# Kernel optimization log

Measured on AMD Instinct MI355X. Metric: run time of the kernel, lower is better.

## Reference

```python
import jax, jax.numpy as jnp
import numpy as np

P = 16; H_IMG = 384; W_IMG = 384; D = 1024
N_LAYERS = 24; DI = 2048; DS = 16; DTR = 64; DC = 4; EPS = 1e-5


def setup_inputs() -> dict:
    key = jax.random.key(0)
    ks = jax.random.split(key, 12)
    B = 2
    inp = {}
    inp["x"] = jax.random.normal(ks[0], (B, 3, H_IMG, W_IMG), jnp.float32)
    inp["patch_w"] = jax.random.normal(ks[1], (D, 3, P, P), jnp.float32) * 0.02
    inp["patch_b"] = jnp.zeros((D,), jnp.float32)
    inp["pos_embed"] = jax.random.normal(ks[2], (1, (H_IMG // P) * (W_IMG // P), D), jnp.float32) * 0.02
    inp["ln_g"] = jnp.ones((N_LAYERS, D), jnp.float32)
    inp["ln_b"] = jnp.zeros((N_LAYERS, D), jnp.float32)
    inp["in_w"] = jax.random.normal(ks[3], (N_LAYERS, 2 * DI, D), jnp.float32) * 0.02
    inp["conv_w"] = jax.random.normal(ks[4], (N_LAYERS, DI, DC), jnp.float32) * 0.1
    inp["conv_b"] = jnp.zeros((N_LAYERS, DI), jnp.float32)
    inp["xproj_w"] = jax.random.normal(ks[5], (N_LAYERS, DTR + 2 * DS, DI), jnp.float32) * 0.02
    inp["dt_w"] = jax.random.normal(ks[6], (N_LAYERS, DI, DTR), jnp.float32) * 0.02
    inp["dt_b"] = jnp.full((N_LAYERS, DI), -4.0, jnp.float32)  # softplus(-4) ~ 0.018
    inp["A_log"] = jnp.broadcast_to(jnp.log(jnp.arange(1, DS + 1, dtype=jnp.float32)), (N_LAYERS, DI, DS)).copy()
    inp["D_param"] = jnp.ones((N_LAYERS, DI), jnp.float32)
    inp["out_w"] = jax.random.normal(ks[7], (N_LAYERS, D, DI), jnp.float32) * 0.02
    return inp


def _layer_norm(x, g, b):
    mu = jnp.mean(x, axis=-1, keepdims=True)
    var = jnp.var(x, axis=-1, keepdims=True)
    return (x - mu) * jax.lax.rsqrt(var + EPS) * g + b


def _mamba_block(x, p):
    g, bn, Win, Wc, bc, Wxp, Wdt, bdt, Alog, Dd, Wout = p
    u = _layer_norm(x, g, bn)                          # [B,L,D]
    xz = jnp.einsum('bld,ed->ble', u, Win)             # [B,L,2*DI]
    xi, z = jnp.split(xz, 2, axis=-1)
    # causal depthwise conv1d along L (kernel DC=4)
    xt = jnp.moveaxis(xi, 1, 2)                        # [B,DI,L]
    L = xt.shape[-1]
    xpad = jnp.pad(xt, ((0, 0), (0, 0), (DC - 1, 0)))
    xc = sum(Wc[:, k][None, :, None] * xpad[:, :, k:k + L] for k in range(DC)) + bc[None, :, None]
    xc = jax.nn.silu(jnp.moveaxis(xc, 1, 2))           # [B,L,DI]
    dbc = jnp.einsum('bld,ed->ble', xc, Wxp)           # [B,L,DTR+2*DS]
    dt, Bm, Cm = jnp.split(dbc, [DTR, DTR + DS], axis=-1)
    dt = jax.nn.softplus(jnp.einsum('blr,dr->bld', dt, Wdt) + bdt)  # [B,L,DI]
    A = -jnp.exp(Alog)                                 # [DI,DS]
    dA = jnp.exp(dt[..., None] * A)                    # [B,L,DI,DS]
    dBx = (dt * xc)[..., None] * Bm[:, :, None, :]     # [B,L,DI,DS]

    def step(h, inp):
        dA_t, dBx_t, C_t = inp
        h = dA_t * h + dBx_t                           # [B,DI,DS]
        y = jnp.einsum('bds,bs->bd', h, C_t)
        return h, y

    h0 = jnp.zeros((x.shape[0], DI, DS), x.dtype)
    xs = (jnp.moveaxis(dA, 1, 0), jnp.moveaxis(dBx, 1, 0), jnp.moveaxis(Cm, 1, 0))
    _, ys = jax.lax.scan(step, h0, xs)                 # ys: [L,B,DI]
    y = jnp.moveaxis(ys, 0, 1) + Dd * xc
    y = y * jax.nn.silu(z)
    return x + jnp.einsum('ble,de->bld', y, Wout)


def _forward(x, patch_w, patch_b, pos_embed, ln_g, ln_b, in_w, conv_w, conv_b,
             xproj_w, dt_w, dt_b, A_log, D_param, out_w):
    feat = jax.lax.conv_general_dilated(
        x, patch_w, (P, P), 'VALID',
        dimension_numbers=('NCHW', 'OIHW', 'NCHW')) + patch_b[None, :, None, None]
    Bn, Dd, Hh, Ww = feat.shape
    tok = feat.reshape(Bn, Dd, Hh * Ww).transpose(0, 2, 1)  # [B,L,D]
    h0, w0 = H_IMG // P, W_IMG // P
    pe = pos_embed.reshape(1, h0, w0, Dd)
    pe = jax.image.resize(pe, (1, Hh, Ww, Dd), 'bilinear')  # align_corners=False
    tok = tok + pe.reshape(1, Hh * Ww, Dd)
    params = (ln_g, ln_b, in_w, conv_w, conv_b, xproj_w, dt_w, dt_b, A_log, D_param, out_w)

    def layer(carry, p):
        return jax.checkpoint(_mamba_block)(carry, p), None

    tok, _ = jax.lax.scan(layer, tok, params)
    return tok


def reference(x, patch_w, patch_b, pos_embed, ln_g, ln_b, in_w, conv_w, conv_b,
              xproj_w, dt_w, dt_b, A_log, D_param, out_w):
    return _forward(x, patch_w, patch_b, pos_embed, ln_g, ln_b, in_w, conv_w, conv_b,
                    xproj_w, dt_w, dt_b, A_log, D_param, out_w)
```

## Files before the change

kernel.cpp:

```cpp
#include <hip/hip_runtime.h>
#include <hip/hip_bf16.h>
#include <math.h>

#define PATCH   16
#define HIMG    384
#define WIMG    384
#define DMODEL  1024
#define NLAYERS 24
#define DI      2048
#define DSTATE  16
#define DTR     64
#define DC      4
#define LN_EPS  1e-5f
#define BATCH   2
#define GRIDTOK 24
#define LTOK    (GRIDTOK*GRIDTOK)
#define NTOK    (BATCH*LTOK)
#define KPATCH  (3*PATCH*PATCH)
#define NCH     16
#define LC      (LTOK/NCH)
#define PSTRIDE ((size_t)NTOK * 2 * DI)
#define XP_SK   16

typedef __attribute__((ext_vector_type(8))) short short8;
typedef __attribute__((ext_vector_type(4))) float f32x4;

__device__ __forceinline__ float sigmoidf_(float v) { return 1.f / (1.f + __expf(-v)); }
__device__ __forceinline__ unsigned short f2bf(float f) {
    __hip_bfloat16 h = __float2bfloat16(f);
    return *(unsigned short*)&h;
}

__device__ __forceinline__ int xcd_swizzle(int orig, int nwg) {
    const int q = nwg >> 3, r = nwg & 7;
    const int xcd = orig & 7, idx = orig >> 3;
    return (xcd < r ? xcd * (q + 1) : r * (q + 1) + (xcd - r) * q) + idx;
}
__device__ __forceinline__ void swz_xyz(int& bx, int& by, int& bz) {
    const int gx = gridDim.x, gy = gridDim.y;
    const int nwg = gx * gy * gridDim.z;
    const int orig = blockIdx.x + gx * (blockIdx.y + gy * blockIdx.z);
    const int id = xcd_swizzle(orig, nwg);
    bx = id % gx;
    const int rest = id / gx;
    by = rest % gy;
    bz = rest / gy;
}

__global__ void f2bf_kernel(const float* __restrict__ in, unsigned short* __restrict__ out, int n4) {
    for (int i = blockIdx.x * blockDim.x + threadIdx.x; i < n4; i += gridDim.x * blockDim.x) {
        const float4 v = ((const float4*)in)[i];
        ushort4 o;
        o.x = f2bf(v.x); o.y = f2bf(v.y); o.z = f2bf(v.z); o.w = f2bf(v.w);
        ((ushort4*)out)[i] = o;
    }
}

__global__ void im2col_kernel(const float* __restrict__ x, unsigned short* __restrict__ xcol) {
    int idx = blockIdx.x * blockDim.x + threadIdx.x;
    if (idx >= NTOK * KPATCH) return;
    int t = idx / KPATCH, k = idx % KPATCH;
    int b = t / LTOK, hw = t % LTOK;
    int h = hw / GRIDTOK, w = hw % GRIDTOK;
    int c = k / (PATCH*PATCH), r = k % (PATCH*PATCH);
    int i = r / PATCH, j = r % PATCH;
    xcol[idx] = f2bf(x[(((size_t)(b*3 + c)*HIMG) + h*PATCH + i)*WIMG + w*PATCH + j]);
}

__global__ __launch_bounds__(256) void layernorm_kernel(
        const float* __restrict__ x, const float* __restrict__ g,
        const float* __restrict__ b, unsigned short* __restrict__ u) {
    const int t = blockIdx.x;
    const int tid = threadIdx.x;
    const float4 xv = ((const float4*)(x + (size_t)t * DMODEL))[tid];
    float s = xv.x + xv.y + xv.z + xv.w;
    float q = xv.x*xv.x + xv.y*xv.y + xv.z*xv.z + xv.w*xv.w;
    #pragma unroll
    for (int off = 32; off >= 1; off >>= 1) {
        s += __shfl_xor(s, off);
        q += __shfl_xor(q, off);
    }
    __shared__ float red[8];
    if ((tid & 63) == 0) { red[tid >> 6] = s; red[4 + (tid >> 6)] = q; }
    __syncthreads();
    s = red[0] + red[1] + red[2] + red[3];
    q = red[4] + red[5] + red[6] + red[7];
    const float mu   = s * (1.f / DMODEL);
    const float var  = q * (1.f / DMODEL) - mu * mu;
    const float rstd = rsqrtf(var + LN_EPS);
    const float4 gv = ((const float4*)g)[tid];
    const float4 bv = ((const float4*)b)[tid];
    ushort4 o;
    o.x = f2bf((xv.x - mu) * rstd * gv.x + bv.x);
    o.y = f2bf((xv.y - mu) * rstd * gv.y + bv.y);
    o.z = f2bf((xv.z - mu) * rstd * gv.z + bv.z);
    o.w = f2bf((xv.w - mu) * rstd * gv.w + bv.w);
    ((ushort4*)(u + (size_t)t * DMODEL))[tid] = o;
}

__global__ __launch_bounds__(256) void gemm_mfma_bt(
        const unsigned short* __restrict__ A, int lda,
        const float* __restrict__ B, int ldb,
        float* __restrict__ C, int M, int N, int Ksub) {
    __shared__ unsigned short As[128 * 64];
    __shared__ unsigned short Bs[128 * 64];
    int bx, by, bz;
    swz_xyz(bx, by, bz);
    const int tid = threadIdx.x;
    const int m0 = bx * 128;
    const int n0 = by * 128;
    const int koff = bz * Ksub;
    C += (size_t)bz * M * N;

    const int lane = tid & 63;
    const int wid  = tid >> 6;
    const int wm = (wid >> 1) * 64;
    const int wn = (wid & 1) * 64;
    const int fr = lane & 15;
    const int cb = lane >> 4;

    const int srow = tid >> 3;
    const int skc  = tid & 7;

    f32x4 acc[4][4];
    #pragma unroll
    for (int i = 0; i < 4; ++i)
        #pragma unroll
        for (int j = 0; j < 4; ++j) acc[i][j] = (f32x4){0.f, 0.f, 0.f, 0.f};

    uint4  areg[4];
    float4 breg[4][2];

    const int nk = Ksub / 64;
    #pragma unroll
    for (int i = 0; i < 4; ++i) {
        const int r = srow + 32 * i;
        areg[i] = *(const uint4*)(A + (size_t)(m0 + r) * lda + koff + skc * 8);
        const float* bp = B + (size_t)(n0 + r) * ldb + koff + skc * 8;
        breg[i][0] = *(const float4*)bp;
        breg[i][1] = *(const float4*)(bp + 4);
    }

    for (int ks = 0; ks < nk; ++ks) {
        __syncthreads();
        #pragma unroll
        for (int i = 0; i < 4; ++i) {
            const int r = srow + 32 * i;
            const int idx = r * 64 + ((skc ^ (r & 7)) << 3);
            *(uint4*)&As[idx] = areg[i];
            const float* bf = (const float*)&breg[i][0];
            short8 hv;
            #pragma unroll
            for (int j = 0; j < 8; ++j) hv[j] = (short)f2bf(bf[j]);
            *(short8*)&Bs[idx] = hv;
        }
        __syncthreads();
        if (ks + 1 < nk) {
            const int k1 = koff + (ks + 1) * 64;
            #pragma unroll
            for (int i = 0; i < 4; ++i) {
                const int r = srow + 32 * i;
                areg[i] = *(const uint4*)(A + (size_t)(m0 + r) * lda + k1 + skc * 8);
                const float* bp = B + (size_t)(n0 + r) * ldb + k1 + skc * 8;
                breg[i][0] = *(const float4*)bp;
                breg[i][1] = *(const float4*)(bp + 4);
            }
        }
        #pragma unroll
        for (int kk = 0; kk < 2; ++kk) {
            short8 af[4], bfr[4];
            #pragma unroll
            for (int mi = 0; mi < 4; ++mi) {
                const int row = wm + mi * 16 + fr;
                af[mi] = *(const short8*)&As[row * 64 + (((kk * 4 + cb) ^ (row & 7)) << 3)];
            }
            #pragma unroll
            for (int ni = 0; ni < 4; ++ni) {
                const int row = wn + ni * 16 + fr;
                bfr[ni] = *(const short8*)&Bs[row * 64 + (((kk * 4 + cb) ^ (row & 7)) << 3)];
            }
            #pragma unroll
            for (int mi = 0; mi < 4; ++mi)
                #pragma unroll
                for (int ni = 0; ni < 4; ++ni)
                    acc[mi][ni] = __builtin_amdgcn_mfma_f32_16x16x32_bf16(
                        af[mi], bfr[ni], acc[mi][ni], 0, 0, 0);
        }
    }

    #pragma unroll
    for (int mi = 0; mi < 4; ++mi) {
        const int rbase = m0 + wm + mi * 16 + cb * 4;
        #pragma unroll
        for (int ni = 0; ni < 4; ++ni) {
            const int col = n0 + wn + ni * 16 + fr;
            #pragma unroll
            for (int j = 0; j < 4; ++j)
                C[(size_t)(rbase + j) * N + col] = acc[mi][ni][j];
        }
    }
}

template<int EPI>
__global__ __launch_bounds__(256) void gemm_bb(
        const unsigned short* __restrict__ A, int lda,
        const unsigned short* __restrict__ B, int ldb,
        float* __restrict__ C, int M, int N, int Ksub,
        const float* __restrict__ bias, const float* __restrict__ aux) {
    __shared__ unsigned short As[128 * 64];
    __shared__ unsigned short Bs[128 * 64];
    int bx, by, bz;
    swz_xyz(bx, by, bz);
    const int tid = threadIdx.x;
    const int m0 = bx * 128;
    const int n0 = by * 128;

    const int lane = tid & 63;
    const int wid  = tid >> 6;
    const int wm = (wid >> 1) * 64;
    const int wn = (wid & 1) * 64;
    const int fr = lane & 15;
    const int cb = lane >> 4;
    const int srow = tid >> 3;
    const int skc  = tid & 7;

    f32x4 acc[4][4];
    #pragma unroll
    for (int i = 0; i < 4; ++i)
        #pragma unroll
        for (int j = 0; j < 4; ++j) acc[i][j] = (f32x4){0.f, 0.f, 0.f, 0.f};

    uint4 areg[4], breg[4];
    const int nk = Ksub / 64;
    #pragma unroll
    for (int i = 0; i < 4; ++i) {
        const int r = srow + 32 * i;
        areg[i] = *(const uint4*)(A + (size_t)(m0 + r) * lda + skc * 8);
        breg[i] = *(const uint4*)(B + (size_t)(n0 + r) * ldb + skc * 8);
    }

    for (int ks = 0; ks < nk; ++ks) {
        __syncthreads();
        #pragma unroll
        for (int i = 0; i < 4; ++i) {
            const int r = srow + 32 * i;
            const int idx = r * 64 + ((skc ^ (r & 7)) << 3);
            *(uint4*)&As[idx] = areg[i];
            *(uint4*)&Bs[idx] = breg[i];
        }
        __syncthreads();
        if (ks + 1 < nk) {
            const int k1 = (ks + 1) * 64;
            #pragma unroll
            for (int i = 0; i < 4; ++i) {
                const int r = srow + 32 * i;
                areg[i] = *(const uint4*)(A + (size_t)(m0 + r) * lda + k1 + skc * 8);
                breg[i] = *(const uint4*)(B + (size_t)(n0 + r) * ldb + k1 + skc * 8);
            }
        }
        #pragma unroll
        for (int kk = 0; kk < 2; ++kk) {
            short8 af[4], bfr[4];
            #pragma unroll
            for (int mi = 0; mi < 4; ++mi) {
                const int row = wm + mi * 16 + fr;
                af[mi] = *(const short8*)&As[row * 64 + (((kk * 4 + cb) ^ (row & 7)) << 3)];
            }
            #pragma unroll
            for (int ni = 0; ni < 4; ++ni) {
                const int row = wn + ni * 16 + fr;
                bfr[ni] = *(const short8*)&Bs[row * 64 + (((kk * 4 + cb) ^ (row & 7)) << 3)];
            }
            #pragma unroll
            for (int mi = 0; mi < 4; ++mi)
                #pragma unroll
                for (int ni = 0; ni < 4; ++ni)
                    acc[mi][ni] = __builtin_amdgcn_mfma_f32_16x16x32_bf16(
                        af[mi], bfr[ni], acc[mi][ni], 0, 0, 0);
        }
    }

    #pragma unroll
    for (int mi = 0; mi < 4; ++mi) {
        const int rbase = m0 + wm + mi * 16 + cb * 4;
        #pragma unroll
        for (int ni = 0; ni < 4; ++ni) {
            const int col = n0 + wn + ni * 16 + fr;
            #pragma unroll
            for (int j = 0; j < 4; ++j) {
                float v = acc[mi][ni][j];
                if (EPI == 2)
                    v += bias[col] + aux[(size_t)((rbase + j) % LTOK) * DMODEL + col];
                C[(size_t)(rbase + j) * N + col] = v;
            }
        }
    }
}

__global__ __launch_bounds__(256) void gemm_xproj64(
        const unsigned short* __restrict__ A,
        const unsigned short* __restrict__ B,
        float* __restrict__ C) {
    __shared__ unsigned short As[64 * 64];
    __shared__ unsigned short Bs[96 * 64];
    int bx, by, bz;
    swz_xyz(bx, by, bz);
    const int tid = threadIdx.x;
    const int m0 = bx * 64;
    const int koff = by * (DI / XP_SK);
    C += (size_t)by * NTOK * 96;

    const int lane = tid & 63;
    const int wid  = tid >> 6;
    const int wm = wid * 16;
    const int fr = lane & 15;
    const int cb = lane >> 4;
    const int srow = tid >> 3;
    const int skc  = tid & 7;

    f32x4 acc[6];
    #pragma unroll
    for (int j = 0; j < 6; ++j) acc[j] = (f32x4){0.f, 0.f, 0.f, 0.f};

    uint4 areg[2], breg[3];
    areg[0] = *(const uint4*)(A + (size_t)(m0 + srow) * DI + koff + skc * 8);
    areg[1] = *(const uint4*)(A + (size_t)(m0 + srow + 32) * DI + koff + skc * 8);
    #pragma unroll
    for (int i = 0; i < 3; ++i) {
        const int idx = tid + 256 * i;
        breg[i] = *(const uint4*)(B + (size_t)(idx >> 3) * DI + koff + (idx & 7) * 8);
    }

    const int nk = (DI / XP_SK) / 64;
    for (int ks = 0; ks < nk; ++ks) {
        __syncthreads();
        {
            const int r0 = srow, r1 = srow + 32;
            *(uint4*)&As[r0 * 64 + ((skc ^ (r0 & 7)) << 3)] = areg[0];
            *(uint4*)&As[r1 * 64 + ((skc ^ (r1 & 7)) << 3)] = areg[1];
        }
        #pragma unroll
        for (int i = 0; i < 3; ++i) {
            const int idx = tid + 256 * i;
            const int r = idx >> 3, kc = idx & 7;
            *(uint4*)&Bs[r * 64 + ((kc ^ (r & 7)) << 3)] = breg[i];
        }
        __syncthreads();
        if (ks + 1 < nk) {
            const int k1 = koff + (ks + 1) * 64;
            areg[0] = *(const uint4*)(A + (size_t)(m0 + srow) * DI + k1 + skc * 8);
            areg[1] = *(const uint4*)(A + (size_t)(m0 + srow + 32) * DI + k1 + skc * 8);
            #pragma unroll
            for (int i = 0; i < 3; ++i) {
                const int idx = tid + 256 * i;
                breg[i] = *(const uint4*)(B + (size_t)(idx >> 3) * DI + k1 + (idx & 7) * 8);
            }
        }
        #pragma unroll
        for (int kk = 0; kk < 2; ++kk) {
            const int arow = wm + fr;
            const short8 af = *(const short8*)&As[arow * 64 + (((kk * 4 + cb) ^ (arow & 7)) << 3)];
            short8 bfr[6];
            #pragma unroll
            for (int ni = 0; ni < 6; ++ni) {
                const int row = ni * 16 + fr;
                bfr[ni] = *(const short8*)&Bs[row * 64 + (((kk * 4 + cb) ^ (row & 7)) << 3)];
            }
            #pragma unroll
            for (int ni = 0; ni < 6; ++ni)
                acc[ni] = __builtin_amdgcn_mfma_f32_16x16x32_bf16(af, bfr[ni], acc[ni], 0, 0, 0);
        }
    }

    const int rbase = m0 + wm + cb * 4;
    #pragma unroll
    for (int ni = 0; ni < 6; ++ni) {
        const int col = ni * 16 + fr;
        #pragma unroll
        for (int j = 0; j < 4; ++j)
            C[(size_t)(rbase + j) * 96 + col] = acc[ni][j];
    }
}

__global__ __launch_bounds__(256) void gemm_dt(
        const unsigned short* __restrict__ A,
        const unsigned short* __restrict__ B,
        float* __restrict__ C, const float* __restrict__ bias) {
    __shared__ unsigned short As[128 * 64];
    __shared__ unsigned short Bs[64 * 64];
    int bx, by, bz;
    swz_xyz(bx, by, bz);
    const int tid = threadIdx.x;
    const int m0 = bx * 128;
    const int n0 = by * 64;

    const int lane = tid & 63;
    const int wid  = tid >> 6;
    const int wm = (wid >> 1) * 64;
    const int wn = (wid & 1) * 32;
    const int fr = lane & 15;
    const int cb = lane >> 4;
    const int srow = tid >> 3;
    const int skc  = tid & 7;

    #pragma unroll
    for (int i = 0; i < 4; ++i) {
        const int r = srow + 32 * i;
        const uint4 v = *(const uint4*)(A + (size_t)(m0 + r) * 64 + skc * 8);
        *(uint4*)&As[r * 64 + ((skc ^ (r & 7)) << 3)] = v;
    }
    #pragma unroll
    for (int i = 0; i < 2; ++i) {
        const int r = srow + 32 * i;
        const uint4 v = *(const uint4*)(B + (size_t)(n0 + r) * 64 + skc * 8);
        *(uint4*)&Bs[r * 64 + ((skc ^ (r & 7)) << 3)] = v;
    }
    __syncthreads();

    f32x4 acc[4][2];
    #pragma unroll
    for (int i = 0; i < 4; ++i)
        #pragma unroll
        for (int j = 0; j < 2; ++j) acc[i][j] = (f32x4){0.f, 0.f, 0.f, 0.f};

    #pragma unroll
    for (int kk = 0; kk < 2; ++kk) {
        short8 af[4], bfr[2];
        #pragma unroll
        for (int mi = 0; mi < 4; ++mi) {
            const int row = wm + mi * 16 + fr;
            af[mi] = *(const short8*)&As[row * 64 + (((kk * 4 + cb) ^ (row & 7)) << 3)];
        }
        #pragma unroll
        for (int ni = 0; ni < 2; ++ni) {
            const int row = wn + ni * 16 + fr;
            bfr[ni] = *(const short8*)&Bs[row * 64 + (((kk * 4 + cb) ^ (row & 7)) << 3)];
        }
        #pragma unroll
        for (int mi = 0; mi < 4; ++mi)
            #pragma unroll
            for (int ni = 0; ni < 2; ++ni)
                acc[mi][ni] = __builtin_amdgcn_mfma_f32_16x16x32_bf16(
                    af[mi], bfr[ni], acc[mi][ni], 0, 0, 0);
    }

    #pragma unroll
    for (int mi = 0; mi < 4; ++mi) {
        const int rbase = m0 + wm + mi * 16 + cb * 4;
        #pragma unroll
        for (int ni = 0; ni < 2; ++ni) {
            const int col = n0 + wn + ni * 16 + fr;
            #pragma unroll
            for (int j = 0; j < 4; ++j) {
                float v = acc[mi][ni][j] + bias[col];
                v = (v > 20.f) ? v : log1pf(__expf(v));
                C[(size_t)(rbase + j) * DI + col] = v;
            }
        }
    }
}

__global__ void reduce16_kernel(const float* __restrict__ part, float* __restrict__ out,
                                unsigned short* __restrict__ out64, int n) {
    int i = blockIdx.x * blockDim.x + threadIdx.x;
    if (i >= n) return;
    float s = 0.f;
    #pragma unroll
    for (int z = 0; z < XP_SK; ++z) s += part[(size_t)z * n + i];
    out[i] = s;
    const int col = i % 96;
    if (col < 64) out64[(i / 96) * 64 + col] = f2bf(s);
}

__global__ void conv1d_silu_kernel(const float* __restrict__ xzP,
                                   const float* __restrict__ wc,
                                   const float* __restrict__ bc,
                                   float* __restrict__ xc,
                                   unsigned short* __restrict__ xc_bf) {
    int idx = blockIdx.x * blockDim.x + threadIdx.x;
    if (idx >= NTOK * DI) return;
    const int t = idx >> 11;
    const int e = idx & (DI - 1);
    const int l = t % LTOK;
    const float4 w = *(const float4*)(wc + e * DC);
    const float* xp0 = xzP + (size_t)t * (2*DI) + e;
    const float* xp1 = xp0 + PSTRIDE;
    float acc = bc[e] + w.w * (xp0[0] + xp1[0]);
    if (l >= 1) acc += w.z * (xp0[-(2*DI)]   + xp1[-(2*DI)]);
    if (l >= 2) acc += w.y * (xp0[-2*(2*DI)] + xp1[-2*(2*DI)]);
    if (l >= 3) acc += w.x * (xp0[-3*(2*DI)] + xp1[-3*(2*DI)]);
    const float r = acc * sigmoidf_(acc);
    xc[idx] = r;
    xc_bf[idx] = f2bf(r);
}

__global__ __launch_bounds__(256) void scan_pass1(
        const float* __restrict__ dt, const float* __restrict__ xc,
        const float* __restrict__ dbc, const float* __restrict__ Alog,
        float* __restrict__ Fst, float* __restrict__ sdt) {
    const int tid = threadIdx.x;
    const int e  = blockIdx.x * 256 + tid;
    const int c  = blockIdx.y;
    const int b  = blockIdx.z;
    const int l0 = c * LC;
    const size_t tb = (size_t)b * LTOK + l0;

    __shared__ float Bs[LC][16];
    for (int idx = tid; idx < LC * 16; idx += 256) {
        const int row = idx >> 4, s = idx & 15;
        Bs[row][s] = dbc[(tb + row) * 96 + 64 + s];
    }

    float Aval[DSTATE];
    {
        const float* ap = Alog + (size_t)e * DSTATE;
        #pragma unroll
        for (int s = 0; s < DSTATE; ++s) Aval[s] = -__expf(ap[s]);
    }
    __syncthreads();

    const float* dtp = dt + tb * DI + e;
    const float* xcp = xc + tb * DI + e;
    float h[DSTATE];
    #pragma unroll
    for (int s = 0; s < DSTATE; ++s) h[s] = 0.f;
    float sum_dt = 0.f;

    float dtv = dtp[0], xcv = xcp[0];
    for (int l = 0; l < LC; ++l) {
        float dtn = 0.f, xcn = 0.f;
        if (l + 1 < LC) { dtn = dtp[(size_t)(l+1) * DI]; xcn = xcp[(size_t)(l+1) * DI]; }
        sum_dt += dtv;
        const float dx = dtv * xcv;
        const float4* brow = (const float4*)&Bs[l][0];
        const float4 b0 = brow[0], b1 = brow[1], b2 = brow[2], b3 = brow[3];
        const float bb[16] = {b0.x,b0.y,b0.z,b0.w, b1.x,b1.y,b1.z,b1.w,
                              b2.x,b2.y,b2.z,b2.w, b3.x,b3.y,b3.z,b3.w};
        #pragma unroll
        for (int s = 0; s < DSTATE; ++s)
            h[s] = fmaf(__expf(dtv * Aval[s]), h[s], dx * bb[s]);
        dtv = dtn; xcv = xcn;
    }

    float4* Fp = (float4*)(Fst + ((((size_t)b * NCH + c) * DI) + e) * DSTATE);
    #pragma unroll
    for (int q = 0; q < 4; ++q)
        Fp[q] = make_float4(h[q*4+0], h[q*4+1], h[q*4+2], h[q*4+3]);
    sdt[((size_t)b * NCH + c) * DI + e] = sum_dt;
}

__global__ __launch_bounds__(256) void scan_pass3(
        const float* __restrict__ dt, const float* __restrict__ xc,
        const float* __restrict__ dbc, const float* __restrict__ xzP,
        const float* __restrict__ Alog, const float* __restrict__ Dp,
        const float* __restrict__ Fst, const float* __restrict__ sdt,
        unsigned short* __restrict__ y) {
    const int tid = threadIdx.x;
    const int e  = blockIdx.x * 256 + tid;
    const int c  = blockIdx.y;
    const int b  = blockIdx.z;
    const int l0 = c * LC;
    const size_t tb = (size_t)b * LTOK + l0;

    __shared__ float BCs[LC][32];
    for (int idx = tid; idx < LC * 32; idx += 256) {
        const int row = idx >> 5, col = idx & 31;
        BCs[row][col] = dbc[(tb + row) * 96 + 64 + col];
    }

    float Aval[DSTATE];
    {
        const float* ap = Alog + (size_t)e * DSTATE;
        #pragma unroll
        for (int s = 0; s < DSTATE; ++s) Aval[s] = -__expf(ap[s]);
    }
    const float Dv = Dp[e];

    float h[DSTATE];
    #pragma unroll
    for (int s = 0; s < DSTATE; ++s) h[s] = 0.f;
    for (int c2 = 0; c2 < c; ++c2) {
        const size_t base = ((size_t)b * NCH + c2) * DI + e;
        const float sd = sdt[base];
        const float4* Fp = (const float4*)(Fst + base * DSTATE);
        const float4 f0 = Fp[0], f1 = Fp[1], f2 = Fp[2], f3 = Fp[3];
        const float ff[16] = {f0.x,f0.y,f0.z,f0.w, f1.x,f1.y,f1.z,f1.w,
                              f2.x,f2.y,f2.z,f2.w, f3.x,f3.y,f3.z,f3.w};
        #pragma unroll
        for (int s = 0; s < DSTATE; ++s)
            h[s] = fmaf(__expf(Aval[s] * sd), h[s], ff[s]);
    }
    __syncthreads();

    const float* dtp = dt + tb * DI + e;
    const float* xcp = xc + tb * DI + e;
    const float* zp0 = xzP + tb * (2*DI) + DI + e;
    const float* zp1 = zp0 + PSTRIDE;
    unsigned short* yp = y + tb * DI + e;

    float dtv = dtp[0], xcv = xcp[0], zv = zp0[0] + zp1[0];
    for (int l = 0; l < LC; ++l) {
        float dtn = 0.f, xcn = 0.f, zn = 0.f;
        if (l + 1 < LC) {
            dtn = dtp[(size_t)(l+1) * DI];
            xcn = xcp[(size_t)(l+1) * DI];
            zn  = zp0[(size_t)(l+1) * (2*DI)] + zp1[(size_t)(l+1) * (2*DI)];
        }
        const float dx = dtv * xcv;
        const float4* brow = (const float4*)&BCs[l][0];
        const float4 b0 = brow[0], b1 = brow[1], b2 = brow[2], b3 = brow[3];
        const float4 c0 = brow[4], c1 = brow[5], c2 = brow[6], c3 = brow[7];
        const float bb[16] = {b0.x,b0.y,b0.z,b0.w, b1.x,b1.y,b1.z,b1.w,
                              b2.x,b2.y,b2.z,b2.w, b3.x,b3.y,b3.z,b3.w};
        const float cc[16] = {c0.x,c0.y,c0.z,c0.w, c1.x,c1.y,c1.z,c1.w,
                              c2.x,c2.y,c2.z,c2.w, c3.x,c3.y,c3.z,c3.w};
        float yv = 0.f;
        #pragma unroll
        for (int s = 0; s < DSTATE; ++s) {
            h[s] = fmaf(__expf(dtv * Aval[s]), h[s], dx * bb[s]);
            yv = fmaf(h[s], cc[s], yv);
        }
        yp[(size_t)l * DI] = f2bf((yv + Dv * xcv) * (zv * sigmoidf_(zv)));
        dtv = dtn; xcv = xcn; zv = zn;
    }
}

template<bool DO_LN>
__global__ __launch_bounds__(256) void reduce8_ln_kernel(
        const float* __restrict__ part, float* __restrict__ tok,
        const float* __restrict__ g, const float* __restrict__ b,
        unsigned short* __restrict__ u) {
    const int t = blockIdx.x;
    const int tid = threadIdx.x;
    const int n4 = NTOK * DMODEL / 4;
    const int i = t * 256 + tid;
    float4 tv = ((float4*)tok)[i];
    #pragma unroll
    for (int z = 0; z < 8; ++z) {
        const float4 p = ((const float4*)part)[(size_t)z * n4 + i];
        tv.x += p.x; tv.y += p.y; tv.z += p.z; tv.w += p.w;
    }
    ((float4*)tok)[i] = tv;
    if (DO_LN) {
        float s = tv.x + tv.y + tv.z + tv.w;
        float q = tv.x*tv.x + tv.y*tv.y + tv.z*tv.z + tv.w*tv.w;
        #pragma unroll
        for (int off = 32; off >= 1; off >>= 1) {
            s += __shfl_xor(s, off);
            q += __shfl_xor(q, off);
        }
        __shared__ float red[8];
        if ((tid & 63) == 0) { red[tid >> 6] = s; red[4 + (tid >> 6)] = q; }
        __syncthreads();
        s = red[0] + red[1] + red[2] + red[3];
        q = red[4] + red[5] + red[6] + red[7];
        const float mu   = s * (1.f / DMODEL);
        const float var  = q * (1.f / DMODEL) - mu * mu;
        const float rstd = rsqrtf(var + LN_EPS);
        const float4 gv = ((const float4*)g)[tid];
        const float4 bv = ((const float4*)b)[tid];
        ushort4 o;
        o.x = f2bf((tv.x - mu) * rstd * gv.x + bv.x);
        o.y = f2bf((tv.y - mu) * rstd * gv.y + bv.y);
        o.z = f2bf((tv.z - mu) * rstd * gv.z + bv.z);
        o.w = f2bf((tv.w - mu) * rstd * gv.w + bv.w);
        ((ushort4*)(u + (size_t)t * DMODEL))[tid] = o;
    }
}

extern "C" void kernel_launch(void* const* d_in, const int* in_sizes, int n_in,
                              void* d_out, int out_size, void* d_ws, size_t ws_size,
                              hipStream_t stream) {
    const float* x       = (const float*)d_in[0];
    const float* patch_w = (const float*)d_in[1];
    const float* patch_b = (const float*)d_in[2];
    const float* pos     = (const float*)d_in[3];
    const float* ln_g    = (const float*)d_in[4];
    const float* ln_b    = (const float*)d_in[5];
    const float* in_w    = (const float*)d_in[6];
    const float* conv_w  = (const float*)d_in[7];
    const float* conv_b  = (const float*)d_in[8];
    const float* xproj_w = (const float*)d_in[9];
    const float* dt_w    = (const float*)d_in[10];
    const float* dt_b    = (const float*)d_in[11];
    const float* A_log   = (const float*)d_in[12];
    const float* D_par   = (const float*)d_in[13];
    const float* out_w   = (const float*)d_in[14];

    float* tok = (float*)d_out;
    float* ws  = (float*)d_ws;
    float* xzP  = ws;  ws += 2 * PSTRIDE;
    float* xc   = ws;  ws += (size_t)NTOK * DI;
    float* dbcP = ws;  ws += (size_t)XP_SK * NTOK * 96;
    float* dbc  = ws;  ws += (size_t)NTOK * 96;
    float* dtb  = ws;  ws += (size_t)NTOK * DI;
    float* Fst  = ws;  ws += (size_t)BATCH * NCH * DI * DSTATE;
    float* sdt  = ws;  ws += (size_t)BATCH * NCH * DI;
    unsigned short* us = (unsigned short*)ws;
    unsigned short* Xcol_bf  = us; us += (size_t)NTOK * KPATCH;
    unsigned short* u_bf     = us; us += (size_t)NTOK * DMODEL;
    unsigned short* xc_bf    = us; us += (size_t)NTOK * DI;
    unsigned short* yb_bf    = us; us += (size_t)NTOK * DI;
    unsigned short* dbc64_bf = us; us += (size_t)NTOK * 64;
    unsigned short* wxpb  = us; us += (size_t)NLAYERS * 96 * DI;
    unsigned short* wdtb  = us; us += (size_t)NLAYERS * DI * DTR;
    unsigned short* wpb   = us; us += (size_t)DMODEL * KPATCH;

    f2bf_kernel<<<1024, 256, 0, stream>>>(xproj_w, wxpb, NLAYERS*96*DI/4);
    f2bf_kernel<<<1024, 256, 0, stream>>>(dt_w,    wdtb, NLAYERS*DI*DTR/4);
    f2bf_kernel<<<256,  256, 0, stream>>>(patch_w, wpb,  DMODEL*KPATCH/4);

    im2col_kernel<<<(NTOK*KPATCH + 255)/256, 256, 0, stream>>>(x, Xcol_bf);
    gemm_bb<2><<<dim3(NTOK/128, DMODEL/128), 256, 0, stream>>>(
        Xcol_bf, KPATCH, wpb, KPATCH, tok, NTOK, DMODEL, KPATCH, patch_b, pos);

    layernorm_kernel<<<NTOK, 256, 0, stream>>>(tok, ln_g, ln_b, u_bf);

    for (int layer = 0; layer < NLAYERS; ++layer) {
        const float* Win = in_w  + (size_t)layer * 2 * DI * DMODEL;
        const float* Wo  = out_w + (size_t)layer * DMODEL * DI;
        const unsigned short* Wxp = wxpb + (size_t)layer * 96 * DI;
        const unsigned short* Wdt = wdtb + (size_t)layer * DI * DTR;
        const float* Wc  = conv_w + (size_t)layer * DI * DC;
        const float* Bc  = conv_b + (size_t)layer * DI;
        const float* Bdt = dt_b   + (size_t)layer * DI;
        const float* Al  = A_log  + (size_t)layer * DI * DSTATE;
        const float* Dd  = D_par  + (size_t)layer * DI;

        gemm_mfma_bt<<<dim3(NTOK/128, (2*DI)/128, 2), 256, 0, stream>>>(
            u_bf, DMODEL, Win, DMODEL, xzP, NTOK, 2*DI, DMODEL/2);
        conv1d_silu_kernel<<<(NTOK*DI + 255)/256, 256, 0, stream>>>(xzP, Wc, Bc, xc, xc_bf);
        gemm_xproj64<<<dim3(NTOK/64, XP_SK), 256, 0, stream>>>(xc_bf, Wxp, dbcP);
        reduce16_kernel<<<(NTOK*96 + 255)/256, 256, 0, stream>>>(dbcP, dbc, dbc64_bf, NTOK*96);
        gemm_dt<<<dim3(NTOK/128, DI/64), 256, 0, stream>>>(dbc64_bf, Wdt, dtb, Bdt);
        scan_pass1<<<dim3(DI/256, NCH, BATCH), 256, 0, stream>>>(
            dtb, xc, dbc, Al, Fst, sdt);
        scan_pass3<<<dim3(DI/256, NCH, BATCH), 256, 0, stream>>>(
            dtb, xc, dbc, xzP, Al, Dd, Fst, sdt, yb_bf);
        gemm_mfma_bt<<<dim3(NTOK/128, DMODEL/128, 8), 256, 0, stream>>>(
            yb_bf, DI, Wo, DI, xzP, NTOK, DMODEL, DI/8);
        if (layer < NLAYERS - 1)
            reduce8_ln_kernel<true><<<NTOK, 256, 0, stream>>>(
                xzP, tok, ln_g + (size_t)(layer+1) * DMODEL, ln_b + (size_t)(layer+1) * DMODEL, u_bf);
        else
            reduce8_ln_kernel<false><<<NTOK, 256, 0, stream>>>(
                xzP, tok, nullptr, nullptr, u_bf);
    }
}
```

Before: 3.961 ms.

## Store in-projection split-K partials as bf16 and double scan chunk count

The in-projection GEMM now writes its two split-K partial outputs in bf16 instead of fp32, and the conv1d and scan pass-3 kernels read those bf16 partials and convert them back to float. This halves the memory traffic of the largest intermediate buffer. The scan is also split into 32 chunks instead of 16 for more parallelism, and pass-3 visits chunks in reverse block order. Rounding the partials to bf16 before summing them loses some accuracy in the x and z activations.

New measurement: 4.002 ms. About the same (+1.0%).

```diff
diff --git a/kernel.cpp b/kernel.cpp
--- a/kernel.cpp
+++ b/kernel.cpp
@@ -17,9 +17,9 @@
 #define LTOK    (GRIDTOK*GRIDTOK)
 #define NTOK    (BATCH*LTOK)
 #define KPATCH  (3*PATCH*PATCH)
-#define NCH     16
+#define NCH     32
 #define LC      (LTOK/NCH)
-#define PSTRIDE ((size_t)NTOK * 2 * DI)
+#define XZPSTRIDE ((size_t)NTOK * 2 * DI)
 #define XP_SK   16
 
 typedef __attribute__((ext_vector_type(8))) short short8;
@@ -30,6 +30,12 @@
     __hip_bfloat16 h = __float2bfloat16(f);
     return *(unsigned short*)&h;
 }
+__device__ __forceinline__ float bf2f(unsigned short v) {
+    unsigned int u = ((unsigned int)v) << 16;
+    return __builtin_bit_cast(float, u);
+}
+__device__ __forceinline__ void storeC(float* p, float v) { *p = v; }
+__device__ __forceinline__ void storeC(unsigned short* p, float v) { *p = f2bf(v); }
 
 __device__ __forceinline__ int xcd_swizzle(int orig, int nwg) {
     const int q = nwg >> 3, r = nwg & 7;
@@ -98,10 +104,11 @@
     ((ushort4*)(u + (size_t)t * DMODEL))[tid] = o;
 }
 
+template<typename OT>
 __global__ __launch_bounds__(256) void gemm_mfma_bt(
         const unsigned short* __restrict__ A, int lda,
         const float* __restrict__ B, int ldb,
-        float* __restrict__ C, int M, int N, int Ksub) {
+        OT* __restrict__ C, int M, int N, int Ksub) {
     __shared__ unsigned short As[128 * 64];
     __shared__ unsigned short Bs[128 * 64];
     int bx, by, bz;
@@ -196,7 +203,7 @@
             const int col = n0 + wn + ni * 16 + fr;
             #pragma unroll
             for (int j = 0; j < 4; ++j)
-                C[(size_t)(rbase + j) * N + col] = acc[mi][ni][j];
+                storeC(&C[(size_t)(rbase + j) * N + col], acc[mi][ni][j]);
         }
     }
 }
@@ -472,7 +479,7 @@
     if (col < 64) out64[(i / 96) * 64 + col] = f2bf(s);
 }
 
-__global__ void conv1d_silu_kernel(const float* __restrict__ xzP,
+__global__ void conv1d_silu_kernel(const unsigned short* __restrict__ xzPb,
                                    const float* __restrict__ wc,
                                    const float* __restrict__ bc,
                                    float* __restrict__ xc,
@@ -483,12 +490,12 @@
     const int e = idx & (DI - 1);
     const int l = t % LTOK;
     const float4 w = *(const float4*)(wc + e * DC);
-    const float* xp0 = xzP + (size_t)t * (2*DI) + e;
-    const float* xp1 = xp0 + PSTRIDE;
-    float acc = bc[e] + w.w * (xp0[0] + xp1[0]);
-    if (l >= 1) acc += w.z * (xp0[-(2*DI)]   + xp1[-(2*DI)]);
-    if (l >= 2) acc += w.y * (xp0[-2*(2*DI)] + xp1[-2*(2*DI)]);
-    if (l >= 3) acc += w.x * (xp0[-3*(2*DI)] + xp1[-3*(2*DI)]);
+    const unsigned short* xp0 = xzPb + (size_t)t * (2*DI) + e;
+    const unsigned short* xp1 = xp0 + XZPSTRIDE;
+    float acc = bc[e] + w.w * (bf2f(xp0[0]) + bf2f(xp1[0]));
+    if (l >= 1) acc += w.z * (bf2f(xp0[-(2*DI)])   + bf2f(xp1[-(2*DI)]));
+    if (l >= 2) acc += w.y * (bf2f(xp0[-2*(2*DI)]) + bf2f(xp1[-2*(2*DI)]));
+    if (l >= 3) acc += w.x * (bf2f(xp0[-3*(2*DI)]) + bf2f(xp1[-3*(2*DI)]));
     const float r = acc * sigmoidf_(acc);
     xc[idx] = r;
     xc_bf[idx] = f2bf(r);
@@ -551,13 +558,13 @@
 
 __global__ __launch_bounds__(256) void scan_pass3(
         const float* __restrict__ dt, const float* __restrict__ xc,
-        const float* __restrict__ dbc, const float* __restrict__ xzP,
+        const float* __restrict__ dbc, const unsigned short* __restrict__ xzPb,
         const float* __restrict__ Alog, const float* __restrict__ Dp,
         const float* __restrict__ Fst, const float* __restrict__ sdt,
         unsigned short* __restrict__ y) {
     const int tid = threadIdx.x;
     const int e  = blockIdx.x * 256 + tid;
-    const int c  = blockIdx.y;
+    const int c  = (NCH - 1) - blockIdx.y;
     const int b  = blockIdx.z;
     const int l0 = c * LC;
     const size_t tb = (size_t)b * LTOK + l0;
@@ -594,17 +601,17 @@
 
     const float* dtp = dt + tb * DI + e;
     const float* xcp = xc + tb * DI + e;
-    const float* zp0 = xzP + tb * (2*DI) + DI + e;
-    const float* zp1 = zp0 + PSTRIDE;
+    const unsigned short* zp0 = xzPb + tb * (2*DI) + DI + e;
+    const unsigned short* zp1 = zp0 + XZPSTRIDE;
     unsigned short* yp = y + tb * DI + e;
 
-    float dtv = dtp[0], xcv = xcp[0], zv = zp0[0] + zp1[0];
+    float dtv = dtp[0], xcv = xcp[0], zv = bf2f(zp0[0]) + bf2f(zp1[0]);
     for (int l = 0; l < LC; ++l) {
         float dtn = 0.f, xcn = 0.f, zn = 0.f;
         if (l + 1 < LC) {
             dtn = dtp[(size_t)(l+1) * DI];
             xcn = xcp[(size_t)(l+1) * DI];
-            zn  = zp0[(size_t)(l+1) * (2*DI)] + zp1[(size_t)(l+1) * (2*DI)];
+            zn  = bf2f(zp0[(size_t)(l+1) * (2*DI)]) + bf2f(zp1[(size_t)(l+1) * (2*DI)]);
         }
         const float dx = dtv * xcv;
         const float4* brow = (const float4*)&BCs[l][0];
@@ -689,7 +696,7 @@
 
     float* tok = (float*)d_out;
     float* ws  = (float*)d_ws;
-    float* xzP  = ws;  ws += 2 * PSTRIDE;
+    float* xzP  = ws;  ws += (size_t)8 * NTOK * DMODEL;
     float* xc   = ws;  ws += (size_t)NTOK * DI;
     float* dbcP = ws;  ws += (size_t)XP_SK * NTOK * 96;
     float* dbc  = ws;  ws += (size_t)NTOK * 96;
@@ -697,6 +704,7 @@
     float* Fst  = ws;  ws += (size_t)BATCH * NCH * DI * DSTATE;
     float* sdt  = ws;  ws += (size_t)BATCH * NCH * DI;
     unsigned short* us = (unsigned short*)ws;
+    unsigned short* xzPb     = us; us += 2 * XZPSTRIDE;
     unsigned short* Xcol_bf  = us; us += (size_t)NTOK * KPATCH;
     unsigned short* u_bf     = us; us += (size_t)NTOK * DMODEL;
     unsigned short* xc_bf    = us; us += (size_t)NTOK * DI;
@@ -727,17 +735,17 @@
         const float* Al  = A_log  + (size_t)layer * DI * DSTATE;
         const float* Dd  = D_par  + (size_t)layer * DI;
 
-        gemm_mfma_bt<<<dim3(NTOK/128, (2*DI)/128, 2), 256, 0, stream>>>(
-            u_bf, DMODEL, Win, DMODEL, xzP, NTOK, 2*DI, DMODEL/2);
-        conv1d_silu_kernel<<<(NTOK*DI + 255)/256, 256, 0, stream>>>(xzP, Wc, Bc, xc, xc_bf);
+        gemm_mfma_bt<unsigned short><<<dim3(NTOK/128, (2*DI)/128, 2), 256, 0, stream>>>(
+            u_bf, DMODEL, Win, DMODEL, xzPb, NTOK, 2*DI, DMODEL/2);
+        conv1d_silu_kernel<<<(NTOK*DI + 255)/256, 256, 0, stream>>>(xzPb, Wc, Bc, xc, xc_bf);
         gemm_xproj64<<<dim3(NTOK/64, XP_SK), 256, 0, stream>>>(xc_bf, Wxp, dbcP);
         reduce16_kernel<<<(NTOK*96 + 255)/256, 256, 0, stream>>>(dbcP, dbc, dbc64_bf, NTOK*96);
         gemm_dt<<<dim3(NTOK/128, DI/64), 256, 0, stream>>>(dbc64_bf, Wdt, dtb, Bdt);
         scan_pass1<<<dim3(DI/256, NCH, BATCH), 256, 0, stream>>>(
             dtb, xc, dbc, Al, Fst, sdt);
         scan_pass3<<<dim3(DI/256, NCH, BATCH), 256, 0, stream>>>(
-            dtb, xc, dbc, xzP, Al, Dd, Fst, sdt, yb_bf);
-        gemm_mfma_bt<<<dim3(NTOK/128, DMODEL/128, 8), 256, 0, stream>>>(
+            dtb, xc, dbc, xzPb, Al, Dd, Fst, sdt, yb_bf);
+        gemm_mfma_bt<float><<<dim3(NTOK/128, DMODEL/128, 8), 256, 0, stream>>>(
             yb_bf, DI, Wo, DI, xzP, NTOK, DMODEL, DI/8);
         if (layer < NLAYERS - 1)
             reduce8_ln_kernel<true><<<NTOK, 256, 0, stream>>>(
```

## Fuse conv1d+SiLU into x-proj GEMM and fold split-K reduction into consumers

Applied to the files above, without the earlier changes.

Computes the causal depthwise conv and SiLU inside the x-projection GEMM's A-tile load, which removes the separate conv kernel and the bf16 xc buffer. It also drops the reduce16 kernel: gemm_dt and both scan passes now sum the 16 split-K partials themselves. This saves two launches per layer and some intermediate traffic. In exchange, the register prefetch double-buffering is gone, and the conv reads 4 shifted rows from both K-partials of xzP. The partial sums are also reduced redundantly in several kernels.

New measurement: 4.008 ms. About the same (+1.2%).

```diff
diff --git a/kernel.cpp b/kernel.cpp
--- a/kernel.cpp
+++ b/kernel.cpp
@@ -297,10 +297,13 @@
     }
 }
 
-__global__ __launch_bounds__(256) void gemm_xproj64(
-        const unsigned short* __restrict__ A,
+__global__ __launch_bounds__(256) void gemm_xproj_conv(
+        const float* __restrict__ xzP,
+        const float* __restrict__ wc,
+        const float* __restrict__ bc,
         const unsigned short* __restrict__ B,
-        float* __restrict__ C) {
+        float* __restrict__ C,
+        float* __restrict__ xc) {
     __shared__ unsigned short As[64 * 64];
     __shared__ unsigned short Bs[96 * 64];
     int bx, by, bz;
@@ -322,40 +325,63 @@
     #pragma unroll
     for (int j = 0; j < 6; ++j) acc[j] = (f32x4){0.f, 0.f, 0.f, 0.f};
 
-    uint4 areg[2], breg[3];
-    areg[0] = *(const uint4*)(A + (size_t)(m0 + srow) * DI + koff + skc * 8);
-    areg[1] = *(const uint4*)(A + (size_t)(m0 + srow + 32) * DI + koff + skc * 8);
-    #pragma unroll
-    for (int i = 0; i < 3; ++i) {
-        const int idx = tid + 256 * i;
-        breg[i] = *(const uint4*)(B + (size_t)(idx >> 3) * DI + koff + (idx & 7) * 8);
-    }
-
     const int nk = (DI / XP_SK) / 64;
     for (int ks = 0; ks < nk; ++ks) {
-        __syncthreads();
-        {
-            const int r0 = srow, r1 = srow + 32;
-            *(uint4*)&As[r0 * 64 + ((skc ^ (r0 & 7)) << 3)] = areg[0];
-            *(uint4*)&As[r1 * 64 + ((skc ^ (r1 & 7)) << 3)] = areg[1];
+        if (ks) __syncthreads();
+        #pragma unroll
+        for (int i = 0; i < 2; ++i) {
+            const int r = srow + 32 * i;
+            const int t = m0 + r;
+            const int l = t % LTOK;
+            const int e0 = koff + ks * 64 + skc * 8;
+            float a[8];
+            {
+                const float4 b0 = *(const float4*)(bc + e0);
+                const float4 b1 = *(const float4*)(bc + e0 + 4);
+                a[0]=b0.x; a[1]=b0.y; a[2]=b0.z; a[3]=b0.w;
+                a[4]=b1.x; a[5]=b1.y; a[6]=b1.z; a[7]=b1.w;
+            }
+            float4 wv[8];
+            #pragma unroll
+            for (int j = 0; j < 8; ++j) wv[j] = *(const float4*)(wc + (size_t)(e0 + j) * DC);
+            #pragma unroll
+            for (int dt_ = 0; dt_ < 4; ++dt_) {
+                if (l >= dt_) {
+                    const float* p0 = xzP + (size_t)(t - dt_) * (2*DI) + e0;
+                    const float* p1 = p0 + PSTRIDE;
+                    const float4 x0 = *(const float4*)p0, x1 = *(const float4*)(p0 + 4);
+                    const float4 y0 = *(const float4*)p1, y1 = *(const float4*)(p1 + 4);
+                    const float sx[8] = {x0.x+y0.x, x0.y+y0.y, x0.z+y0.z, x0.w+y0.w,
+                                         x1.x+y1.x, x1.y+y1.y, x1.z+y1.z, x1.w+y1.w};
+                    #pragma unroll
+                    for (int j = 0; j < 8; ++j) {
+                        const float wk = (dt_ == 0) ? wv[j].w : (dt_ == 1) ? wv[j].z
+                                       : (dt_ == 2) ? wv[j].y : wv[j].x;
+                        a[j] = fmaf(wk, sx[j], a[j]);
+                    }
+                }
+            }
+            short8 hv;
+            float4 o0, o1;
+            #pragma unroll
+            for (int j = 0; j < 8; ++j) {
+                const float rv = a[j] * sigmoidf_(a[j]);
+                hv[j] = (short)f2bf(rv);
+                if (j < 4) ((float*)&o0)[j] = rv; else ((float*)&o1)[j-4] = rv;
+            }
+            float* xp = xc + (size_t)t * DI + e0;
+            *(float4*)xp = o0;
+            *(float4*)(xp + 4) = o1;
+            *(short8*)&As[r * 64 + ((skc ^ (r & 7)) << 3)] = hv;
         }
         #pragma unroll
         for (int i = 0; i < 3; ++i) {
             const int idx = tid + 256 * i;
             const int r = idx >> 3, kc = idx & 7;
-            *(uint4*)&Bs[r * 64 + ((kc ^ (r & 7)) << 3)] = breg[i];
+            const uint4 v = *(const uint4*)(B + (size_t)r * DI + koff + ks * 64 + kc * 8);
+            *(uint4*)&Bs[r * 64 + ((kc ^ (r & 7)) << 3)] = v;
         }
         __syncthreads();
-        if (ks + 1 < nk) {
-            const int k1 = koff + (ks + 1) * 64;
-            areg[0] = *(const uint4*)(A + (size_t)(m0 + srow) * DI + k1 + skc * 8);
-            areg[1] = *(const uint4*)(A + (size_t)(m0 + srow + 32) * DI + k1 + skc * 8);
-            #pragma unroll
-            for (int i = 0; i < 3; ++i) {
-                const int idx = tid + 256 * i;
-                breg[i] = *(const uint4*)(B + (size_t)(idx >> 3) * DI + k1 + (idx & 7) * 8);
-            }
-        }
         #pragma unroll
         for (int kk = 0; kk < 2; ++kk) {
             const int arow = wm + fr;
@@ -383,7 +409,7 @@
 }
 
 __global__ __launch_bounds__(256) void gemm_dt(
-        const unsigned short* __restrict__ A,
+        const float* __restrict__ dbcP,
         const unsigned short* __restrict__ B,
         float* __restrict__ C, const float* __restrict__ bias) {
     __shared__ unsigned short As[128 * 64];
@@ -406,8 +432,19 @@
     #pragma unroll
     for (int i = 0; i < 4; ++i) {
         const int r = srow + 32 * i;
-        const uint4 v = *(const uint4*)(A + (size_t)(m0 + r) * 64 + skc * 8);
-        *(uint4*)&As[r * 64 + ((skc ^ (r & 7)) << 3)] = v;
+        const int t = m0 + r;
+        const float* pb = dbcP + (size_t)t * 96 + skc * 8;
+        float s[8] = {0.f,0.f,0.f,0.f,0.f,0.f,0.f,0.f};
+        for (int z = 0; z < XP_SK; ++z) {
+            const float4 v0 = *(const float4*)(pb + (size_t)z * NTOK * 96);
+            const float4 v1 = *(const float4*)(pb + (size_t)z * NTOK * 96 + 4);
+            s[0]+=v0.x; s[1]+=v0.y; s[2]+=v0.z; s[3]+=v0.w;
+            s[4]+=v1.x; s[5]+=v1.y; s[6]+=v1.z; s[7]+=v1.w;
+        }
+        short8 hv;
+        #pragma unroll
+        for (int j = 0; j < 8; ++j) hv[j] = (short)f2bf(s[j]);
+        *(short8*)&As[r * 64 + ((skc ^ (r & 7)) << 3)] = hv;
     }
     #pragma unroll
     for (int i = 0; i < 2; ++i) {
@@ -460,43 +497,9 @@
     }
 }
 
-__global__ void reduce16_kernel(const float* __restrict__ part, float* __restrict__ out,
-                                unsigned short* __restrict__ out64, int n) {
-    int i = blockIdx.x * blockDim.x + threadIdx.x;
-    if (i >= n) return;
-    float s = 0.f;
-    #pragma unroll
-    for (int z = 0; z < XP_SK; ++z) s += part[(size_t)z * n + i];
-    out[i] = s;
-    const int col = i % 96;
-    if (col < 64) out64[(i / 96) * 64 + col] = f2bf(s);
-}
-
-__global__ void conv1d_silu_kernel(const float* __restrict__ xzP,
-                                   const float* __restrict__ wc,
-                                   const float* __restrict__ bc,
-                                   float* __restrict__ xc,
-                                   unsigned short* __restrict__ xc_bf) {
-    int idx = blockIdx.x * blockDim.x + threadIdx.x;
-    if (idx >= NTOK * DI) return;
-    const int t = idx >> 11;
-    const int e = idx & (DI - 1);
-    const int l = t % LTOK;
-    const float4 w = *(const float4*)(wc + e * DC);
-    const float* xp0 = xzP + (size_t)t * (2*DI) + e;
-    const float* xp1 = xp0 + PSTRIDE;
-    float acc = bc[e] + w.w * (xp0[0] + xp1[0]);
-    if (l >= 1) acc += w.z * (xp0[-(2*DI)]   + xp1[-(2*DI)]);
-    if (l >= 2) acc += w.y * (xp0[-2*(2*DI)] + xp1[-2*(2*DI)]);
-    if (l >= 3) acc += w.x * (xp0[-3*(2*DI)] + xp1[-3*(2*DI)]);
-    const float r = acc * sigmoidf_(acc);
-    xc[idx] = r;
-    xc_bf[idx] = f2bf(r);
-}
-
 __global__ __launch_bounds__(256) void scan_pass1(
         const float* __restrict__ dt, const float* __restrict__ xc,
-        const float* __restrict__ dbc, const float* __restrict__ Alog,
+        const float* __restrict__ dbcP, const float* __restrict__ Alog,
         float* __restrict__ Fst, float* __restrict__ sdt) {
     const int tid = threadIdx.x;
     const int e  = blockIdx.x * 256 + tid;
@@ -508,7 +511,11 @@
     __shared__ float Bs[LC][16];
     for (int idx = tid; idx < LC * 16; idx += 256) {
         const int row = idx >> 4, s = idx & 15;
-        Bs[row][s] = dbc[(tb + row) * 96 + 64 + s];
+        float v = 0.f;
+        const float* p = dbcP + (tb + row) * 96 + 64 + s;
+        #pragma unroll
+        for (int z = 0; z < XP_SK; ++z) v += p[(size_t)z * NTOK * 96];
+        Bs[row][s] = v;
     }
 
     float Aval[DSTATE];
@@ -551,7 +558,7 @@
 
 __global__ __launch_bounds__(256) void scan_pass3(
         const float* __restrict__ dt, const float* __restrict__ xc,
-        const float* __restrict__ dbc, const float* __restrict__ xzP,
+        const float* __restrict__ dbcP, const float* __restrict__ xzP,
         const float* __restrict__ Alog, const float* __restrict__ Dp,
         const float* __restrict__ Fst, const float* __restrict__ sdt,
         unsigned short* __restrict__ y) {
@@ -565,7 +572,11 @@
     __shared__ float BCs[LC][32];
     for (int idx = tid; idx < LC * 32; idx += 256) {
         const int row = idx >> 5, col = idx & 31;
-        BCs[row][col] = dbc[(tb + row) * 96 + 64 + col];
+        float v = 0.f;
+        const float* p = dbcP + (tb + row) * 96 + 64 + col;
+        #pragma unroll
+        for (int z = 0; z < XP_SK; ++z) v += p[(size_t)z * NTOK * 96];
+        BCs[row][col] = v;
     }
 
     float Aval[DSTATE];
@@ -692,16 +703,13 @@
     float* xzP  = ws;  ws += 2 * PSTRIDE;
     float* xc   = ws;  ws += (size_t)NTOK * DI;
     float* dbcP = ws;  ws += (size_t)XP_SK * NTOK * 96;
-    float* dbc  = ws;  ws += (size_t)NTOK * 96;
     float* dtb  = ws;  ws += (size_t)NTOK * DI;
     float* Fst  = ws;  ws += (size_t)BATCH * NCH * DI * DSTATE;
     float* sdt  = ws;  ws += (size_t)BATCH * NCH * DI;
     unsigned short* us = (unsigned short*)ws;
     unsigned short* Xcol_bf  = us; us += (size_t)NTOK * KPATCH;
     unsigned short* u_bf     = us; us += (size_t)NTOK * DMODEL;
-    unsigned short* xc_bf    = us; us += (size_t)NTOK * DI;
     unsigned short* yb_bf    = us; us += (size_t)NTOK * DI;
-    unsigned short* dbc64_bf = us; us += (size_t)NTOK * 64;
     unsigned short* wxpb  = us; us += (size_t)NLAYERS * 96 * DI;
     unsigned short* wdtb  = us; us += (size_t)NLAYERS * DI * DTR;
     unsigned short* wpb   = us; us += (size_t)DMODEL * KPATCH;
@@ -729,14 +737,13 @@
 
         gemm_mfma_bt<<<dim3(NTOK/128, (2*DI)/128, 2), 256, 0, stream>>>(
             u_bf, DMODEL, Win, DMODEL, xzP, NTOK, 2*DI, DMODEL/2);
-        conv1d_silu_kernel<<<(NTOK*DI + 255)/256, 256, 0, stream>>>(xzP, Wc, Bc, xc, xc_bf);
-        gemm_xproj64<<<dim3(NTOK/64, XP_SK), 256, 0, stream>>>(xc_bf, Wxp, dbcP);
-        reduce16_kernel<<<(NTOK*96 + 255)/256, 256, 0, stream>>>(dbcP, dbc, dbc64_bf, NTOK*96);
-        gemm_dt<<<dim3(NTOK/128, DI/64), 256, 0, stream>>>(dbc64_bf, Wdt, dtb, Bdt);
+        gemm_xproj_conv<<<dim3(NTOK/64, XP_SK), 256, 0, stream>>>(
+            xzP, Wc, Bc, Wxp, dbcP, xc);
+        gemm_dt<<<dim3(NTOK/128, DI/64), 256, 0, stream>>>(dbcP, Wdt, dtb, Bdt);
         scan_pass1<<<dim3(DI/256, NCH, BATCH), 256, 0, stream>>>(
-            dtb, xc, dbc, Al, Fst, sdt);
+            dtb, xc, dbcP, Al, Fst, sdt);
         scan_pass3<<<dim3(DI/256, NCH, BATCH), 256, 0, stream>>>(
-            dtb, xc, dbc, xzP, Al, Dd, Fst, sdt, yb_bf);
+            dtb, xc, dbcP, xzP, Al, Dd, Fst, sdt, yb_bf);
         gemm_mfma_bt<<<dim3(NTOK/128, DMODEL/128, 8), 256, 0, stream>>>(
             yb_bf, DI, Wo, DI, xzP, NTOK, DMODEL, DI/8);
         if (layer < NLAYERS - 1)
```
